# Optimization experiments

Measured on AMD Instinct MI355X. Metric: run time of the kernel, lower is better.

## Reference

```python
import jax, jax.numpy as jnp
import numpy as np

LN_EPS = 1e-5


def _ln(h, g, b):
    mu = h.mean(-1, keepdims=True)
    var = ((h - mu) ** 2).mean(-1, keepdims=True)
    return (h - mu) / jnp.sqrt(var + LN_EPS) * g + b


def setup_inputs() -> dict:
    key = jax.random.key(0)
    ks = jax.random.split(key, 12)
    B, T, Cin, C, D, M = 16, 1024, 512, 1024, 256, 1024
    s = 0.02
    inp = {
        "x": jax.random.normal(ks[0], (B, T, Cin), jnp.float32),
        "masks": jnp.ones((B, T), jnp.float32),
        "W1": jax.random.normal(ks[1], (Cin, C), jnp.float32) * s,
        "g1": jnp.ones((C,), jnp.float32), "b1": jnp.zeros((C,), jnp.float32),
        "W2": jax.random.normal(ks[2], (C, C), jnp.float32) * s,
        "g2": jnp.ones((C,), jnp.float32), "b2": jnp.zeros((C,), jnp.float32),
        "W3": jax.random.normal(ks[3], (C, C), jnp.float32) * s,
        "g3": jnp.ones((C,), jnp.float32), "b3": jnp.zeros((C,), jnp.float32),
        "W4": jax.random.normal(ks[4], (C, C), jnp.float32) * s,
        "g4": jnp.ones((C,), jnp.float32), "b4": jnp.zeros((C,), jnp.float32),
        "W5": jax.random.normal(ks[5], (C, D), jnp.float32) * s,
        "b5": jnp.zeros((D,), jnp.float32),
        # Dirichlet(alpha=100) rows, as in the torch init: rows live on the simplex
        "embedding": jax.random.dirichlet(ks[6], jnp.full((D,), 100.0, jnp.float32), (M,)).astype(jnp.float32),
    }
    return inp


def reference(x, masks, W1, g1, b1, W2, g2, b2, W3, g3, b3, W4, g4, b4, W5, b5, embedding):
    h = jax.nn.relu(_ln(x @ W1, g1, b1))
    h = jax.nn.relu(_ln(h @ W2, g2, b2))
    h = jax.nn.relu(_ln(h @ W3, g3, b3))
    h = jax.nn.relu(_ln(h @ W4, g4, b4))
    z = h @ W5 + b5                              # [B, T, D]
    p = jax.nn.log_softmax(z, axis=-1)           # log-prob features

    B, T, D = p.shape
    p_flat = jax.lax.stop_gradient(p.reshape(-1, D))   # x.detach() in torch
    ep = jnp.exp(p_flat)                               # [N, D]
    # KL(exp(p) || e_m) summed over D, for all codes m:
    #   sum_d exp(p)*(p - log(e_m)) = rowsum(exp(p)*p) - exp(p) @ log(E)^T
    div = (ep * p_flat).sum(-1, keepdims=True) - ep @ jnp.log(embedding).T  # [N, M]
    idx = jnp.argmin(div, axis=-1)                     # [N]
    quant = jax.lax.stop_gradient(embedding[idx].reshape(B, T, D))

    # commitment loss: masked KL(exp(p) || quant.detach())
    kl = (jnp.exp(p) * (p - jnp.log(quant))).sum(-1)   # [B, T]
    loss = 0.25 * (kl * masks).mean(0).sum()

    # straight-through estimator
    q = p + jax.lax.stop_gradient(quant - p)
    return z, q, loss
```

## Files before the change

### kernel.cpp

```cpp
#include <hip/hip_runtime.h>
#include <hip/hip_bf16.h>
#include <stdint.h>

typedef __attribute__((ext_vector_type(4))) float f32x4;
typedef __attribute__((ext_vector_type(2))) float f32x2;
typedef __attribute__((ext_vector_type(8))) __bf16 bf16x8;
typedef __attribute__((ext_vector_type(4))) __bf16 bf16x4;

#define LN_EPS 1e-5f

__device__ __forceinline__ void gload_lds16(const void* g, void* l) {
  __builtin_amdgcn_global_load_lds(
      (__attribute__((address_space(1))) void*)(uintptr_t)g,
      (__attribute__((address_space(3))) void*)(uint32_t)(uintptr_t)l,
      16, 0, 0);
}

__device__ __forceinline__ f32x4 mfma16(bf16x8 a, bf16x8 b, f32x4 c) {
  return __builtin_amdgcn_mfma_f32_16x16x32_bf16(a, b, c, 0, 0, 0);
}

__device__ __forceinline__ void transpose256(const float* __restrict__ W,
                                             __bf16* __restrict__ Wt, int K, int N,
                                             int nt, int kt, float (*t)[33]) {
  int tx = threadIdx.x & 31;
  int ty0 = (threadIdx.x >> 5) * 4;
#pragma unroll
  for (int j = 0; j < 4; ++j)
    t[ty0 + j][tx] = W[(size_t)(kt + ty0 + j) * N + nt + tx];
  __syncthreads();
#pragma unroll
  for (int j = 0; j < 4; ++j)
    Wt[(size_t)(nt + ty0 + j) * K + kt + tx] = (__bf16)t[tx][ty0 + j];
}

__global__ __launch_bounds__(256) void k_prep(
    const float* __restrict__ W1, __bf16* __restrict__ W1t,
    const float* __restrict__ W2, __bf16* __restrict__ W2t,
    const float* __restrict__ W3, __bf16* __restrict__ W3t,
    const float* __restrict__ W4, __bf16* __restrict__ W4t,
    const float* __restrict__ W5, __bf16* __restrict__ W5t,
    const float* __restrict__ emb, __bf16* __restrict__ logE) {
  __shared__ float t[32][33];
  const int b = blockIdx.x;
  if (b < 512) {
    transpose256(W1, W1t, 512, 1024, (b & 31) * 32, (b >> 5) * 32, t);
  } else if (b < 3584) {
    int b3 = b - 512;
    int z = b3 >> 10;
    int b4 = b3 & 1023;
    const float* W = z == 0 ? W2 : (z == 1 ? W3 : W4);
    __bf16* T = z == 0 ? W2t : (z == 1 ? W3t : W4t);
    transpose256(W, T, 1024, 1024, (b4 & 31) * 32, (b4 >> 5) * 32, t);
  } else if (b < 3840) {
    int b5 = b - 3584;
    transpose256(W5, W5t, 1024, 256, (b5 & 7) * 32, (b5 >> 3) * 32, t);
  } else {
    int i = (b - 3840) * 256 + threadIdx.x;
    logE[i] = (__bf16)logf(emb[i] * 256.0f);
  }
}

__device__ __forceinline__ void stats_epilogue(char* lds, f32x4 (&acc)[8][4],
                                               f32x2* __restrict__ outPart,
                                               int bm0) {
  const int tid = threadIdx.x;
  const int lane = tid & 63;
  const int wid = tid >> 6;
  const int wm = wid >> 2, wn = wid & 3;
  const int r0 = (lane >> 4) * 4;
  const int cc = lane & 15;
  __builtin_amdgcn_s_barrier();
  float* stp = (float*)lds;
  float* stq = (float*)(lds + 4096);
#pragma unroll
  for (int mi = 0; mi < 8; ++mi) {
#pragma unroll
    for (int j = 0; j < 4; ++j) {
      float s = 0.f, q = 0.f;
#pragma unroll
      for (int ni = 0; ni < 4; ++ni) {
        float v = acc[mi][ni][j];
        s += v; q += v * v;
      }
#pragma unroll
      for (int d = 1; d < 16; d <<= 1) { s += __shfl_xor(s, d); q += __shfl_xor(q, d); }
      if (cc == 0) {
        int rl = wm * 128 + mi * 16 + r0 + j;
        stp[rl * 4 + wn] = s;
        stq[rl * 4 + wn] = q;
      }
    }
  }
  __syncthreads();
  if (tid < 256) {
    float s = stp[tid * 4] + stp[tid * 4 + 1] + stp[tid * 4 + 2] + stp[tid * 4 + 3];
    float q = stq[tid * 4] + stq[tid * 4 + 1] + stq[tid * 4 + 2] + stq[tid * 4 + 3];
    f32x2 pr; pr[0] = s; pr[1] = q;
    outPart[(size_t)(bm0 + tid) * 4 + blockIdx.y] = pr;
  }
}

__device__ __forceinline__ void gemm256_core(
    const __bf16* __restrict__ A, const __bf16* __restrict__ Bt,
    char* lds, int bm0, int bn0, int K, f32x4 (&acc)[8][4]) {
  const int tid = threadIdx.x;
  const int lane = tid & 63;
  const int wid = tid >> 6;
  const int wm = wid >> 2;
  const int wn = wid & 3;
  const int NT = K >> 6;

  const int slin = tid * 16;
  const int lrow = slin >> 7;
  const int scol = (slin & 127) ^ ((lrow & 7) << 4);
  const char* Ab = (const char*)A;
  const char* Bb = (const char*)Bt;
  const uint32_t rs = (uint32_t)K * 2;

  const int klo = (lane >> 4) * 16;
  const int sw = (lane & 7) << 4;
  const uint32_t kx0 = (uint32_t)(klo ^ sw);
  const uint32_t kx1 = (uint32_t)((64 + klo) ^ sw);
  const uint32_t abase = (uint32_t)(wm * 128 + (lane & 15)) * 128;
  const uint32_t bbase = (uint32_t)(wn * 64 + (lane & 15)) * 128;

#pragma unroll
  for (int i = 0; i < 8; ++i)
#pragma unroll
    for (int j = 0; j < 4; ++j) acc[i][j] = 0.0f;

#define LDSA(buf) (lds + (buf)*32768)
#define LDSB(buf) (lds + 65536 + (buf)*32768)
#define STAGE_A(t, h)                                                              \
  {                                                                                \
    const char* src = Ab + (size_t)(bm0 + (h)*128 + lrow) * rs + ((t) << 7) + scol;\
    char* dst = LDSA((t)&1) + (h)*16384 + slin;                                    \
    gload_lds16(src, dst);                                                         \
    gload_lds16(src + (size_t)64 * rs, dst + 8192);                                \
  }
#define STAGE_B(t, h)                                                              \
  {                                                                                \
    const char* src = Bb + (size_t)(bn0 + (h)*128 + lrow) * rs + ((t) << 7) + scol;\
    char* dst = LDSB((t)&1) + (h)*16384 + slin;                                    \
    gload_lds16(src, dst);                                                         \
    gload_lds16(src + (size_t)64 * rs, dst + 8192);                                \
  }
#define HALF1(Acur, Bcur)                                                          \
  _Pragma("unroll") for (int ni = 0; ni < 4; ++ni) {                               \
    bF[ni][0] = *(const bf16x8*)((Bcur) + bbase + ni * 2048 + kx0);                \
    bF[ni][1] = *(const bf16x8*)((Bcur) + bbase + ni * 2048 + kx1);                \
  }                                                                                \
  {                                                                                \
    bf16x8 aF[4][2];                                                               \
    _Pragma("unroll") for (int mi = 0; mi < 4; ++mi) {                             \
      aF[mi][0] = *(const bf16x8*)((Acur) + abase + mi * 2048 + kx0);              \
      aF[mi][1] = *(const bf16x8*)((Acur) + abase + mi * 2048 + kx1);              \
    }                                                                              \
    __builtin_amdgcn_s_setprio(1);                                                 \
    _Pragma("unroll") for (int mi = 0; mi < 4; ++mi)                               \
        _Pragma("unroll") for (int ni = 0; ni < 4; ++ni) {                         \
          acc[mi][ni] = mfma16(aF[mi][0], bF[ni][0], acc[mi][ni]);                 \
          acc[mi][ni] = mfma16(aF[mi][1], bF[ni][1], acc[mi][ni]);                 \
        }                                                                          \
    __builtin_amdgcn_s_setprio(0);                                                 \
  }
#define HALF2(Acur)                                                                \
  {                                                                                \
    bf16x8 aF[4][2];                                                               \
    _Pragma("unroll") for (int mi = 0; mi < 4; ++mi) {                             \
      aF[mi][0] = *(const bf16x8*)((Acur) + abase + (mi + 4) * 2048 + kx0);        \
      aF[mi][1] = *(const bf16x8*)((Acur) + abase + (mi + 4) * 2048 + kx1);        \
    }                                                                              \
    __builtin_amdgcn_s_setprio(1);                                                 \
    _Pragma("unroll") for (int mi = 0; mi < 4; ++mi)                               \
        _Pragma("unroll") for (int ni = 0; ni < 4; ++ni) {                         \
          acc[mi + 4][ni] = mfma16(aF[mi][0], bF[ni][0], acc[mi + 4][ni]);         \
          acc[mi + 4][ni] = mfma16(aF[mi][1], bF[ni][1], acc[mi + 4][ni]);         \
        }                                                                          \
    __builtin_amdgcn_s_setprio(0);                                                 \
  }

  STAGE_A(0, 0); STAGE_A(0, 1); STAGE_B(0, 0); STAGE_B(0, 1);
  STAGE_B(1, 0); STAGE_B(1, 1);
  asm volatile("s_waitcnt vmcnt(4)");
  __builtin_amdgcn_s_barrier();
  __builtin_amdgcn_sched_barrier(0);

  bf16x8 bF[4][2];
  for (int t = 0; t < NT - 2; ++t) {
    const char* Acur = LDSA(t & 1);
    const char* Bcur = LDSB(t & 1);
    STAGE_A(t + 1, 0); STAGE_A(t + 1, 1);
    HALF1(Acur, Bcur)
    __builtin_amdgcn_s_barrier();
    __builtin_amdgcn_sched_barrier(0);
    STAGE_B(t + 2, 0); STAGE_B(t + 2, 1);
    HALF2(Acur)
    asm volatile("s_waitcnt vmcnt(4)");
    __builtin_amdgcn_s_barrier();
    __builtin_amdgcn_sched_barrier(0);
  }
  {
    const char* Acur = LDSA((NT - 2) & 1);
    const char* Bcur = LDSB((NT - 2) & 1);
    STAGE_A(NT - 1, 0); STAGE_A(NT - 1, 1);
    HALF1(Acur, Bcur)
    __builtin_amdgcn_s_barrier();
    __builtin_amdgcn_sched_barrier(0);
    HALF2(Acur)
    asm volatile("s_waitcnt vmcnt(0)");
    __builtin_amdgcn_s_barrier();
    __builtin_amdgcn_sched_barrier(0);
  }
  {
    const char* Acur = LDSA((NT - 1) & 1);
    const char* Bcur = LDSB((NT - 1) & 1);
    HALF1(Acur, Bcur)
    HALF2(Acur)
  }
#undef STAGE_A
#undef HALF1
#undef HALF2
#undef LDSA
#undef LDSB
#undef STAGE_B
}

__global__ __launch_bounds__(512, 2) void k_gemm256_div(
    const __bf16* __restrict__ A, const __bf16* __restrict__ Bt,
    float* __restrict__ part_val, int* __restrict__ part_idx, int N, int K) {
  __shared__ char lds[131072];
  const int bm0 = blockIdx.x * 256;
  const int bn0 = blockIdx.y * 256;
  f32x4 acc[8][4];
  gemm256_core(A, Bt, lds, bm0, bn0, K, acc);

  const int lane = threadIdx.x & 63;
  const int wid = threadIdx.x >> 6;
  const int wm = wid >> 2, wn = wid & 3;
  const int r0 = (lane >> 4) * 4;
  const int cc = lane & 15;
  const int nch = N >> 6;
  const int chunk = (bn0 >> 6) + wn;
#pragma unroll
  for (int mi = 0; mi < 8; ++mi) {
#pragma unroll
    for (int j = 0; j < 4; ++j) {
      float v = acc[mi][0][j];
      int c = cc;
#pragma unroll
      for (int ni = 1; ni < 4; ++ni) {
        float v2 = acc[mi][ni][j];
        int c2 = ni * 16 + cc;
        if (v2 > v) { v = v2; c = c2; }
      }
#pragma unroll
      for (int d = 1; d < 16; d <<= 1) {
        float ov = __shfl_xor(v, d);
        int oc = __shfl_xor(c, d);
        if (ov > v || (ov == v && oc < c)) { v = ov; c = oc; }
      }
      if (cc == 0) {
        int r = bm0 + wm * 128 + mi * 16 + r0 + j;
        part_val[r * nch + chunk] = v;
        part_idx[r * nch + chunk] = bn0 + wn * 64 + c;
      }
    }
  }
}

__global__ __launch_bounds__(512, 2) void k_gemm256_cvt(
    const float* __restrict__ A, const __bf16* __restrict__ Bt,
    __bf16* __restrict__ O, f32x2* __restrict__ outPart, int N, int K) {
  __shared__ char lds[131072];
  const int tid = threadIdx.x;
  const int lane = tid & 63;
  const int wid = tid >> 6;
  const int wm = wid >> 2;
  const int wn = wid & 3;
  const int bm0 = blockIdx.x * 256;
  const int bn0 = blockIdx.y * 256;
  const int NT = K >> 6;

  const int slin = tid * 16;
  const int lrow = slin >> 7;
  const int scol = (slin & 127) ^ ((lrow & 7) << 4);
  const char* Ab = (const char*)A;
  const char* Bb = (const char*)Bt;
  const uint32_t rsA = (uint32_t)K * 4;
  const uint32_t rs = (uint32_t)K * 2;

  const int klo = (lane >> 4) * 16;
  const int sw = (lane & 7) << 4;
  const uint32_t kx0 = (uint32_t)(klo ^ sw);
  const uint32_t kx1 = (uint32_t)((64 + klo) ^ sw);
  const uint32_t abase = (uint32_t)(wm * 128 + (lane & 15)) * 128;
  const uint32_t bbase = (uint32_t)(wn * 64 + (lane & 15)) * 128;

  const int alrow = tid >> 3;
  const uint32_t acolbF = (uint32_t)(tid & 7) * 32;
  const uint32_t awcol = ((uint32_t)(tid & 7) * 16) ^ (uint32_t)((alrow & 7) << 4);
  f32x4 arf[4][2];

  f32x4 acc[8][4];
#pragma unroll
  for (int i = 0; i < 8; ++i)
#pragma unroll
    for (int j = 0; j < 4; ++j) acc[i][j] = 0.0f;

#define LDSA(buf) (lds + (buf)*32768)
#define LDSB(buf) (lds + 65536 + (buf)*32768)
#define STAGE_B(t, h)                                                              \
  {                                                                                \
    const char* src = Bb + (size_t)(bn0 + (h)*128 + lrow) * rs + ((t) << 7) + scol;\
    char* dst = LDSB((t)&1) + (h)*16384 + slin;                                    \
    gload_lds16(src, dst);                                                         \
    gload_lds16(src + (size_t)64 * rs, dst + 8192);                                \
  }
#define A_ISSUE(t1)                                                               \
  {                                                                               \
    const char* base_ = Ab + (size_t)(bm0 + alrow) * rsA + ((size_t)(t1) << 8) + acolbF; \
    _Pragma("unroll") for (int i = 0; i < 4; ++i) {                               \
      arf[i][0] = *(const f32x4*)(base_ + (size_t)(i * 64) * rsA);                \
      arf[i][1] = *(const f32x4*)(base_ + (size_t)(i * 64) * rsA + 16);           \
    }                                                                             \
  }
#define A_WRITE(t1)                                                               \
  {                                                                               \
    char* wb_ = LDSA((t1)&1);                                                     \
    _Pragma("unroll") for (int i = 0; i < 4; ++i) {                               \
      bf16x8 o;                                                                   \
      _Pragma("unroll") for (int e = 0; e < 4; ++e) {                             \
        o[e] = (__bf16)arf[i][0][e];                                              \
        o[e + 4] = (__bf16)arf[i][1][e];                                          \
      }                                                                           \
      *(bf16x8*)(wb_ + (i >> 1) * 16384 + (alrow + (i & 1) * 64) * 128 + awcol) = o; \
    }                                                                             \
  }
#define HALF1(Acur, Bcur)                                                          \
  _Pragma("unroll") for (int ni = 0; ni < 4; ++ni) {                               \
    bF[ni][0] = *(const bf16x8*)((Bcur) + bbase + ni * 2048 + kx0);                \
    bF[ni][1] = *(const bf16x8*)((Bcur) + bbase + ni * 2048 + kx1);                \
  }                                                                                \
  {                                                                                \
    bf16x8 aF[4][2];                                                               \
    _Pragma("unroll") for (int mi = 0; mi < 4; ++mi) {                             \
      aF[mi][0] = *(const bf16x8*)((Acur) + abase + mi * 2048 + kx0);              \
      aF[mi][1] = *(const bf16x8*)((Acur) + abase + mi * 2048 + kx1);              \
    }                                                                              \
    __builtin_amdgcn_s_setprio(1);                                                 \
    _Pragma("unroll") for (int mi = 0; mi < 4; ++mi)                               \
        _Pragma("unroll") for (int ni = 0; ni < 4; ++ni) {                         \
          acc[mi][ni] = mfma16(aF[mi][0], bF[ni][0], acc[mi][ni]);                 \
          acc[mi][ni] = mfma16(aF[mi][1], bF[ni][1], acc[mi][ni]);                 \
        }                                                                          \
    __builtin_amdgcn_s_setprio(0);                                                 \
  }
#define HALF2(Acur)                                                                \
  {                                                                                \
    bf16x8 aF[4][2];                                                               \
    _Pragma("unroll") for (int mi = 0; mi < 4; ++mi) {                             \
      aF[mi][0] = *(const bf16x8*)((Acur) + abase + (mi + 4) * 2048 + kx0);        \
      aF[mi][1] = *(const bf16x8*)((Acur) + abase + (mi + 4) * 2048 + kx1);        \
    }                                                                              \
    __builtin_amdgcn_s_setprio(1);                                                 \
    _Pragma("unroll") for (int mi = 0; mi < 4; ++mi)                               \
        _Pragma("unroll") for (int ni = 0; ni < 4; ++ni) {                         \
          acc[mi + 4][ni] = mfma16(aF[mi][0], bF[ni][0], acc[mi + 4][ni]);         \
          acc[mi + 4][ni] = mfma16(aF[mi][1], bF[ni][1], acc[mi + 4][ni]);         \
        }                                                                          \
    __builtin_amdgcn_s_setprio(0);                                                 \
  }

  A_ISSUE(0)
  STAGE_B(0, 0); STAGE_B(0, 1); STAGE_B(1, 0); STAGE_B(1, 1);
  asm volatile("s_waitcnt vmcnt(8)");
  A_WRITE(0)
  asm volatile("s_waitcnt vmcnt(4) lgkmcnt(0)");
  __builtin_amdgcn_s_barrier();
  __builtin_amdgcn_sched_barrier(0);

  bf16x8 bF[4][2];
  for (int t = 0; t < NT - 2; ++t) {
    const char* Acur = LDSA(t & 1);
    const char* Bcur = LDSB(t & 1);
    A_ISSUE(t + 1)
    HALF1(Acur, Bcur)
    __builtin_amdgcn_s_barrier();
    __builtin_amdgcn_sched_barrier(0);
    STAGE_B(t + 2, 0); STAGE_B(t + 2, 1);
    HALF2(Acur)
    asm volatile("s_waitcnt vmcnt(4)");
    A_WRITE(t + 1)
    asm volatile("s_waitcnt lgkmcnt(0)");
    __builtin_amdgcn_s_barrier();
    __builtin_amdgcn_sched_barrier(0);
  }
  {
    const char* Acur = LDSA((NT - 2) & 1);
    const char* Bcur = LDSB((NT - 2) & 1);
    A_ISSUE(NT - 1)
    HALF1(Acur, Bcur)
    __builtin_amdgcn_s_barrier();
    __builtin_amdgcn_sched_barrier(0);
    HALF2(Acur)
    asm volatile("s_waitcnt vmcnt(0)");
    A_WRITE(NT - 1)
    asm volatile("s_waitcnt lgkmcnt(0)");
    __builtin_amdgcn_s_barrier();
    __builtin_amdgcn_sched_barrier(0);
  }
  {
    const char* Acur = LDSA((NT - 1) & 1);
    const char* Bcur = LDSB((NT - 1) & 1);
    HALF1(Acur, Bcur)
    HALF2(Acur)
  }
#undef STAGE_B
#undef A_ISSUE
#undef A_WRITE
#undef HALF1
#undef HALF2
#undef LDSA
#undef LDSB

  stats_epilogue(lds, acc, outPart, bm0);

  const int r0 = (lane >> 4) * 4;
  const int cc = lane & 15;
#pragma unroll
  for (int mi = 0; mi < 8; ++mi) {
#pragma unroll
    for (int ni = 0; ni < 4; ++ni) {
      int r = bm0 + wm * 128 + mi * 16 + r0;
      int c = bn0 + wn * 64 + ni * 16 + cc;
#pragma unroll
      for (int j = 0; j < 4; ++j)
        O[(size_t)(r + j) * N + c] = (__bf16)acc[mi][ni][j];
    }
  }
}

__global__ __launch_bounds__(512, 2) void k_gemm256_ln(
    const __bf16* __restrict__ A, const __bf16* __restrict__ Bt,
    __bf16* __restrict__ O, const float* __restrict__ gw,
    const float* __restrict__ bw, const f32x2* __restrict__ inPart,
    f32x2* __restrict__ outPart, int N, int K) {
  __shared__ char lds[139264];
  const int GB = 131072;
  const int tid = threadIdx.x;
  const int lane = tid & 63;
  const int wid = tid >> 6;
  const int wm = wid >> 2;
  const int wn = wid & 3;
  const int bm0 = blockIdx.x * 256;
  const int bn0 = blockIdx.y * 256;
  const int NT = K >> 6;

  const int slin = tid * 16;
  const int lrow = slin >> 7;
  const int scol = (slin & 127) ^ ((lrow & 7) << 4);
  const char* Ab = (const char*)A;
  const char* Bb = (const char*)Bt;
  const uint32_t rs = (uint32_t)K * 2;

  const int klo = (lane >> 4) * 16;
  const int sw = (lane & 7) << 4;
  const uint32_t kx0 = (uint32_t)(klo ^ sw);
  const uint32_t kx1 = (uint32_t)((64 + klo) ^ sw);
  const uint32_t abase = (uint32_t)(wm * 128 + (lane & 15)) * 128;
  const uint32_t bbase = (uint32_t)(wn * 64 + (lane & 15)) * 128;

  const int alrow = tid >> 3;
  const uint32_t acolb = (uint32_t)(tid & 7) * 16;
  const uint32_t awcol = acolb ^ (uint32_t)((alrow & 7) << 4);
  float aS[4], cS[4];
  bf16x8 ar[4];

  f32x4 acc[8][4];
#pragma unroll
  for (int i = 0; i < 8; ++i)
#pragma unroll
    for (int j = 0; j < 4; ++j) acc[i][j] = 0.0f;

#define LDSA(buf) (lds + (buf)*32768)
#define LDSB(buf) (lds + 65536 + (buf)*32768)
#define STAGE_B(t, h)                                                              \
  {                                                                                \
    const char* src = Bb + (size_t)(bn0 + (h)*128 + lrow) * rs + ((t) << 7) + scol;\
    char* dst = LDSB((t)&1) + (h)*16384 + slin;                                    \
    gload_lds16(src, dst);                                                         \
    gload_lds16(src + (size_t)64 * rs, dst + 8192);                                \
  }
#define A_ISSUE(t1)                                                               \
  {                                                                               \
    const char* base_ = Ab + (size_t)(bm0 + alrow) * rs + ((size_t)(t1) << 7) + acolb; \
    ar[0] = *(const bf16x8*)(base_);                                              \
    ar[1] = *(const bf16x8*)(base_ + (size_t)64 * rs);                            \
    ar[2] = *(const bf16x8*)(base_ + (size_t)128 * rs);                           \
    ar[3] = *(const bf16x8*)(base_ + (size_t)192 * rs);                           \
  }
#define A_WRITE(t1)                                                               \
  {                                                                               \
    uint32_t gb_ = GB + (uint32_t)(t1)*256 + (uint32_t)(tid & 7) * 32;            \
    f32x4 g0 = *(const f32x4*)(lds + gb_), g1 = *(const f32x4*)(lds + gb_ + 16);  \
    f32x4 b0 = *(const f32x4*)(lds + gb_ + 4096), b1 = *(const f32x4*)(lds + gb_ + 4112); \
    char* wb_ = LDSA((t1)&1);                                                     \
    _Pragma("unroll") for (int i = 0; i < 4; ++i) {                               \
      bf16x8 v = ar[i], o;                                                        \
      _Pragma("unroll") for (int e = 0; e < 8; ++e) {                             \
        float xv = (float)v[e];                                                   \
        float tt = fmaf(xv, aS[i], cS[i]);                                        \
        float ge = e < 4 ? g0[e] : g1[e - 4];                                     \
        float be = e < 4 ? b0[e] : b1[e - 4];                                     \
        tt = fmaf(tt, ge, be);                                                    \
        o[e] = (__bf16)fmaxf(tt, 0.f);                                            \
      }                                                                           \
      *(bf16x8*)(wb_ + (i >> 1) * 16384 + (alrow + (i & 1) * 64) * 128 + awcol) = o; \
    }                                                                             \
  }

  if (tid < 256) {
    ((f32x4*)(lds + GB))[tid] = ((const f32x4*)gw)[tid];
    ((f32x4*)(lds + GB + 4096))[tid] = ((const f32x4*)bw)[tid];
  }
#pragma unroll
  for (int i = 0; i < 4; ++i) {
    int r = bm0 + (i >> 1) * 128 + (i & 1) * 64 + alrow;
    const f32x4* pp = (const f32x4*)(inPart + (size_t)r * 4);
    f32x4 p0 = pp[0], p1 = pp[1];
    float s = p0[0] + p0[2] + p1[0] + p1[2];
    float q = p0[1] + p0[3] + p1[1] + p1[3];
    float mu = s * (1.0f / 1024.0f);
    float var = q * (1.0f / 1024.0f) - mu * mu;
    float rstd = rsqrtf(var + LN_EPS);
    aS[i] = rstd;
    cS[i] = -mu * rstd;
  }
  __builtin_amdgcn_sched_barrier(0);
  A_ISSUE(0)
  STAGE_B(0, 0); STAGE_B(0, 1); STAGE_B(1, 0); STAGE_B(1, 1);
  __builtin_amdgcn_sched_barrier(0);
  asm volatile("s_waitcnt lgkmcnt(0)");
  __builtin_amdgcn_s_barrier();
  asm volatile("s_waitcnt vmcnt(8)");
  A_WRITE(0)
  asm volatile("s_waitcnt vmcnt(4) lgkmcnt(0)");
  __builtin_amdgcn_s_barrier();
  __builtin_amdgcn_sched_barrier(0);

  for (int t = 0; t < NT; ++t) {
    const char* Acur = LDSA(t & 1);
    const char* Bcur = LDSB(t & 1);

    if (t + 1 < NT) { A_ISSUE(t + 1) }
    bf16x8 bF[4][2];
#pragma unroll
    for (int ni = 0; ni < 4; ++ni) {
      bF[ni][0] = *(const bf16x8*)(Bcur + bbase + ni * 2048 + kx0);
      bF[ni][1] = *(const bf16x8*)(Bcur + bbase + ni * 2048 + kx1);
    }
    {
      bf16x8 aF[4][2];
#pragma unroll
      for (int mi = 0; mi < 4; ++mi) {
        aF[mi][0] = *(const bf16x8*)(Acur + abase + mi * 2048 + kx0);
        aF[mi][1] = *(const bf16x8*)(Acur + abase + mi * 2048 + kx1);
      }
      __builtin_amdgcn_s_setprio(1);
#pragma unroll
      for (int mi = 0; mi < 4; ++mi)
#pragma unroll
        for (int ni = 0; ni < 4; ++ni) {
          acc[mi][ni] = mfma16(aF[mi][0], bF[ni][0], acc[mi][ni]);
          acc[mi][ni] = mfma16(aF[mi][1], bF[ni][1], acc[mi][ni]);
        }
      __builtin_amdgcn_s_setprio(0);
    }
    __builtin_amdgcn_s_barrier();
    __builtin_amdgcn_sched_barrier(0);

    if (t + 2 < NT) { STAGE_B(t + 2, 0); STAGE_B(t + 2, 1); }
    {
      bf16x8 aF[4][2];
#pragma unroll
      for (int mi = 0; mi < 4; ++mi) {
        aF[mi][0] = *(const bf16x8*)(Acur + abase + (mi + 4) * 2048 + kx0);
        aF[mi][1] = *(const bf16x8*)(Acur + abase + (mi + 4) * 2048 + kx1);
      }
      __builtin_amdgcn_s_setprio(1);
#pragma unroll
      for (int mi = 0; mi < 4; ++mi)
#pragma unroll
        for (int ni = 0; ni < 4; ++ni) {
          acc[mi + 4][ni] = mfma16(aF[mi][0], bF[ni][0], acc[mi + 4][ni]);
          acc[mi + 4][ni] = mfma16(aF[mi][1], bF[ni][1], acc[mi + 4][ni]);
        }
      __builtin_amdgcn_s_setprio(0);
    }
    if (t + 1 < NT) {
      if (t + 2 < NT) { asm volatile("s_waitcnt vmcnt(4)"); }
      else            { asm volatile("s_waitcnt vmcnt(0)"); }
      A_WRITE(t + 1)
      asm volatile("s_waitcnt lgkmcnt(0)");
      __builtin_amdgcn_s_barrier();
      __builtin_amdgcn_sched_barrier(0);
    }
  }
#undef STAGE_B
#undef A_ISSUE
#undef A_WRITE
#undef LDSA
#undef LDSB

  stats_epilogue(lds, acc, outPart, bm0);

  const int r0 = (lane >> 4) * 4;
  const int cc = lane & 15;
#pragma unroll
  for (int mi = 0; mi < 8; ++mi) {
#pragma unroll
    for (int ni = 0; ni < 4; ++ni) {
      int r = bm0 + wm * 128 + mi * 16 + r0;
      int c = bn0 + wn * 64 + ni * 16 + cc;
#pragma unroll
      for (int j = 0; j < 4; ++j)
        O[(size_t)(r + j) * N + c] = (__bf16)acc[mi][ni][j];
    }
  }
}

__global__ __launch_bounds__(256) void k_gemm_sm(
    const __bf16* __restrict__ A, const __bf16* __restrict__ Bt,
    const float* __restrict__ gw, const float* __restrict__ bw,
    const f32x2* __restrict__ inPart, const float* __restrict__ bias,
    float* __restrict__ z, __bf16* __restrict__ ep, float* __restrict__ sm) {
  const int K = 1024;
  __shared__ char lds[49152];
  const int GBS = 40960;
  char* ldsA = lds;
  char* ldsB = lds + 8192;
  const int tid = threadIdx.x;
  const int lane = tid & 63;
  const int wn = tid >> 6;
  const int bm0 = blockIdx.x * 64;
  const char* Ab = (const char*)A;
  const char* Bb = (const char*)Bt;
  const uint32_t rs = (uint32_t)K * 2;
  const int cc = lane & 15;

  ((f32x4*)(lds + GBS))[tid] = ((const f32x4*)gw)[tid];
  ((f32x4*)(lds + GBS + 4096))[tid] = ((const f32x4*)bw)[tid];

  const int ar0 = tid >> 3;
  float aS[2], cS[2];
#pragma unroll
  for (int i = 0; i < 2; ++i) {
    int r = bm0 + ar0 + i * 32;
    const f32x4* pp = (const f32x4*)(inPart + (size_t)r * 4);
    f32x4 p0 = pp[0], p1 = pp[1];
    float s = p0[0] + p0[2] + p1[0] + p1[2];
    float q = p0[1] + p0[3] + p1[1] + p1[3];
    float mu = s * (1.0f / 1024.0f);
    float var = q * (1.0f / 1024.0f) - mu * mu;
    float rstd = rsqrtf(var + LN_EPS);
    aS[i] = rstd; cS[i] = -mu * rstd;
  }
  const uint32_t acolb = (uint32_t)(tid & 7) * 16;
  const uint32_t awcol = acolb ^ (uint32_t)((ar0 & 7) << 4);

  uint32_t ra[2][4], rb[2][4];
  {
    const int sww = (lane & 7) << 4;
    const int gk = lane & 48;
#pragma unroll
    for (int kk = 0; kk < 2; ++kk) {
#pragma unroll
      for (int i = 0; i < 4; ++i) {
        uint32_t kb = (uint32_t)((kk * 64 + gk) ^ sww);
        ra[kk][i] = (uint32_t)(i * 16 + cc) * 128 + kb;
        rb[kk][i] = (uint32_t)(wn * 64 + i * 16 + cc) * 128 + kb;
      }
    }
  }

  f32x4 acc[4][4];
#pragma unroll
  for (int i = 0; i < 4; ++i)
#pragma unroll
    for (int j = 0; j < 4; ++j) acc[i][j] = 0.0f;

  for (int k0 = 0; k0 < K; k0 += 64) {
    __syncthreads();
    const char* abase_ = Ab + (size_t)(bm0 + ar0) * rs + (size_t)k0 * 2 + acolb;
    bf16x8 a0 = *(const bf16x8*)abase_;
    bf16x8 a1 = *(const bf16x8*)(abase_ + (size_t)32 * rs);
#pragma unroll
    for (int i = 0; i < 8; ++i) {
      int lin = i * 4096 + tid * 16;
      int row = lin >> 7;
      int col = (lin & 127) ^ ((row & 7) << 4);
      gload_lds16(Bb + (size_t)row * rs + k0 * 2 + col, ldsB + lin);
    }
    asm volatile("s_waitcnt vmcnt(8)");
    {
      uint32_t gb_ = GBS + (uint32_t)k0 * 4 + (uint32_t)(tid & 7) * 32;
      f32x4 g0 = *(const f32x4*)(lds + gb_), g1 = *(const f32x4*)(lds + gb_ + 16);
      f32x4 b0 = *(const f32x4*)(lds + gb_ + 4096), b1 = *(const f32x4*)(lds + gb_ + 4112);
      bf16x8 o0, o1;
#pragma unroll
      for (int e = 0; e < 8; ++e) {
        float ge = e < 4 ? g0[e] : g1[e - 4];
        float be = e < 4 ? b0[e] : b1[e - 4];
        float t0 = fmaf(fmaf((float)a0[e], aS[0], cS[0]), ge, be);
        float t1 = fmaf(fmaf((float)a1[e], aS[1], cS[1]), ge, be);
        o0[e] = (__bf16)fmaxf(t0, 0.f);
        o1[e] = (__bf16)fmaxf(t1, 0.f);
      }
      *(bf16x8*)(ldsA + ar0 * 128 + awcol) = o0;
      *(bf16x8*)(ldsA + (ar0 + 32) * 128 + awcol) = o1;
    }
    __syncthreads();
#pragma unroll
    for (int kk = 0; kk < 2; ++kk) {
      bf16x8 af[4], bfv[4];
#pragma unroll
      for (int i = 0; i < 4; ++i) af[i] = *(const bf16x8*)(ldsA + ra[kk][i]);
#pragma unroll
      for (int i = 0; i < 4; ++i) bfv[i] = *(const bf16x8*)(ldsB + rb[kk][i]);
#pragma unroll
      for (int mi = 0; mi < 4; ++mi)
#pragma unroll
        for (int ni = 0; ni < 4; ++ni)
          acc[mi][ni] = mfma16(af[mi], bfv[ni], acc[mi][ni]);
    }
  }

  __syncthreads();
  float* stm = (float*)lds;
  float* sts = (float*)(lds + 1024);
  float* rowm = (float*)(lds + 2048);
  float* rows_ = (float*)(lds + 2304);

  const int r0 = (lane >> 4) * 4;
  float bvv[4];
#pragma unroll
  for (int ni = 0; ni < 4; ++ni) bvv[ni] = bias[wn * 64 + ni * 16 + cc];

#pragma unroll
  for (int mi = 0; mi < 4; ++mi) {
#pragma unroll
    for (int j = 0; j < 4; ++j) {
      float m = -3.4e38f;
#pragma unroll
      for (int ni = 0; ni < 4; ++ni) m = fmaxf(m, acc[mi][ni][j] + bvv[ni]);
#pragma unroll
      for (int d = 1; d < 16; d <<= 1) m = fmaxf(m, __shfl_xor(m, d));
      if (cc == 0) stm[wn * 64 + mi * 16 + r0 + j] = m;
    }
  }
  __syncthreads();
  if (tid < 64) {
    float m = fmaxf(fmaxf(stm[tid], stm[64 + tid]), fmaxf(stm[128 + tid], stm[192 + tid]));
    rowm[tid] = m;
  }
  __syncthreads();
#pragma unroll
  for (int mi = 0; mi < 4; ++mi) {
#pragma unroll
    for (int j = 0; j < 4; ++j) {
      int r = mi * 16 + r0 + j;
      float m = rowm[r];
      float s = 0.f;
#pragma unroll
      for (int ni = 0; ni < 4; ++ni) s += expf(acc[mi][ni][j] + bvv[ni] - m);
#pragma unroll
      for (int d = 1; d < 16; d <<= 1) s += __shfl_xor(s, d);
      if (cc == 0) sts[wn * 64 + r] = s;
    }
  }
  __syncthreads();
  if (tid < 64) {
    float s = sts[tid] + sts[64 + tid] + sts[128 + tid] + sts[192 + tid];
    rows_[tid] = s;
    sm[bm0 + tid] = rowm[tid] + logf(s);
  }
  __syncthreads();
#pragma unroll
  for (int mi = 0; mi < 4; ++mi) {
#pragma unroll
    for (int j = 0; j < 4; ++j) {
      int r = mi * 16 + r0 + j;
      float m = rowm[r];
      float inv = 1.0f / rows_[r];
      float* zp = z + (size_t)(bm0 + r) * 256;
      __bf16* epp = ep + (size_t)(bm0 + r) * 256;
#pragma unroll
      for (int ni = 0; ni < 4; ++ni) {
        int c = wn * 64 + ni * 16 + cc;
        float zz = acc[mi][ni][j] + bvv[ni];
        zp[c] = zz;
        epp[c] = (__bf16)(expf(zz - m) * inv);
      }
    }
  }
}

__global__ __launch_bounds__(256) void k_final(
    const float* __restrict__ part_val, const int* __restrict__ part_idx,
    const float* __restrict__ z, const float* __restrict__ sm,
    const float* __restrict__ emb, const float* __restrict__ masks,
    float* __restrict__ q, float* __restrict__ blockloss) {
  __shared__ float ls[4];
  int lane = threadIdx.x & 63;
  int w = threadIdx.x >> 6;
  int row = blockIdx.x * 4 + w;
  float v = -3.4e38f;
  int c = 0x7fffffff;
  if (lane < 16) { v = part_val[row * 16 + lane]; c = part_idx[row * 16 + lane]; }
#pragma unroll
  for (int d = 1; d < 16; d <<= 1) {
    float ov = __shfl_xor(v, d);
    int oc = __shfl_xor(c, d);
    if (ov > v || (ov == v && oc < c)) { v = ov; c = oc; }
  }
  int code = __shfl(c, 0);
  f32x4 ev = ((const f32x4*)(emb + (size_t)code * 256))[lane];
  ((f32x4*)(q + (size_t)row * 256))[lane] = ev;
  f32x4 zv = ((const f32x4*)(z + (size_t)row * 256))[lane];
  float smr = sm[row];
  float kl = 0.f;
#pragma unroll
  for (int j = 0; j < 4; ++j) {
    float pj = zv[j] - smr;
    kl += expf(pj) * (pj - logf(ev[j]));
  }
#pragma unroll
  for (int d = 1; d < 64; d <<= 1) kl += __shfl_xor(kl, d);
  if (lane == 0) ls[w] = kl * masks[row];
  __syncthreads();
  if (threadIdx.x == 0) blockloss[blockIdx.x] = ls[0] + ls[1] + ls[2] + ls[3];
}

__global__ __launch_bounds__(256) void k_loss_reduce(const float* __restrict__ bl,
                                                     float* __restrict__ out) {
  __shared__ float s[256];
  float a = 0.f;
#pragma unroll
  for (int i = 0; i < 16; ++i) a += bl[threadIdx.x + i * 256];
  s[threadIdx.x] = a;
  __syncthreads();
  for (int st = 128; st > 0; st >>= 1) {
    if (threadIdx.x < st) s[threadIdx.x] += s[threadIdx.x + st];
    __syncthreads();
  }
  if (threadIdx.x == 0) out[0] = s[0] * (0.25f / 16.0f);
}

extern "C" void kernel_launch(void* const* d_in, const int* in_sizes, int n_in,
                              void* d_out, int out_size, void* d_ws, size_t ws_size,
                              hipStream_t stream) {
  const float* x = (const float*)d_in[0];
  const float* masks = (const float*)d_in[1];
  const float* W1 = (const float*)d_in[2];
  const float* g1 = (const float*)d_in[3];
  const float* b1 = (const float*)d_in[4];
  const float* W2 = (const float*)d_in[5];
  const float* g2 = (const float*)d_in[6];
  const float* b2 = (const float*)d_in[7];
  const float* W3 = (const float*)d_in[8];
  const float* g3 = (const float*)d_in[9];
  const float* b3 = (const float*)d_in[10];
  const float* W4 = (const float*)d_in[11];
  const float* g4 = (const float*)d_in[12];
  const float* b4 = (const float*)d_in[13];
  const float* W5 = (const float*)d_in[14];
  const float* b5 = (const float*)d_in[15];
  const float* emb = (const float*)d_in[16];

  const int M = 16384;
  char* ws = (char*)d_ws;
  __bf16* bufA = (__bf16*)(ws);
  __bf16* bufB = (__bf16*)(ws + (32ull << 20));
  __bf16* W1t = (__bf16*)(ws + (64ull << 20));
  __bf16* W2t = (__bf16*)(ws + (65ull << 20));
  __bf16* W3t = (__bf16*)(ws + (67ull << 20));
  __bf16* W4t = (__bf16*)(ws + (69ull << 20));
  __bf16* W5t = (__bf16*)(ws + (71ull << 20));
  __bf16* logE = (__bf16*)(ws + (72ull << 20));
  float* part_val = (float*)(ws + (73ull << 20));
  int* part_idx = (int*)(ws + (74ull << 20));
  float* blockloss = (float*)(ws + (75ull << 20));
  float* sm = (float*)(ws + (76ull << 20));
  f32x2* partA = (f32x2*)(ws + (77ull << 20));
  f32x2* partB = (f32x2*)(ws + (78ull << 20));
  __bf16* ep = (__bf16*)(ws + (16ull << 20));

  float* z = (float*)d_out;
  float* q = z + (size_t)M * 256;
  float* lossp = z + 2ull * M * 256;

  k_prep<<<4864, 256, 0, stream>>>(W1, W1t, W2, W2t, W3, W3t, W4, W4t,
                                   W5, W5t, emb, logE);
  k_gemm256_cvt<<<dim3(64, 4), 512, 0, stream>>>(x, W1t, bufA, partA, 1024, 512);
  k_gemm256_ln<<<dim3(64, 4), 512, 0, stream>>>(bufA, W2t, bufB, g1, b1, partA, partB, 1024, 1024);
  k_gemm256_ln<<<dim3(64, 4), 512, 0, stream>>>(bufB, W3t, bufA, g2, b2, partB, partA, 1024, 1024);
  k_gemm256_ln<<<dim3(64, 4), 512, 0, stream>>>(bufA, W4t, bufB, g3, b3, partA, partB, 1024, 1024);
  k_gemm_sm<<<256, 256, 0, stream>>>(bufB, W5t, g4, b4, partB, b5, z, ep, sm);
  k_gemm256_div<<<dim3(64, 4), 512, 0, stream>>>(ep, logE, part_val, part_idx, 1024, 256);
  k_final<<<4096, 256, 0, stream>>>(part_val, part_idx, z, sm, emb, masks, q, blockloss);
  k_loss_reduce<<<1, 256, 0, stream>>>(blockloss, lossp);
}
```

Before: 247.9 us.

## Double-buffer B tiles in softmax GEMM and fold loss reduce into final kernel

The W5 GEMM kernel now keeps two LDS buffers for the B tile and prefetches tile t+1 while computing tile t, replacing the per-iteration syncthreads pattern with explicit barriers. This hides global-to-LDS latency at the cost of more LDS (80KB), which may lower occupancy. Separately, the final kernel uses an atomic counter so the last block does the loss reduction, removing one kernel launch. The counter is reset in the prep kernel.

```diff
diff --git a/kernel.cpp b/kernel.cpp
--- a/kernel.cpp
+++ b/kernel.cpp
@@ -40,9 +40,11 @@
     const float* __restrict__ W3, __bf16* __restrict__ W3t,
     const float* __restrict__ W4, __bf16* __restrict__ W4t,
     const float* __restrict__ W5, __bf16* __restrict__ W5t,
-    const float* __restrict__ emb, __bf16* __restrict__ logE) {
+    const float* __restrict__ emb, __bf16* __restrict__ logE,
+    int* __restrict__ counter) {
   __shared__ float t[32][33];
   const int b = blockIdx.x;
+  if (b == 0 && threadIdx.x == 0) *counter = 0;
   if (b < 512) {
     transpose256(W1, W1t, 512, 1024, (b & 31) * 32, (b >> 5) * 32, t);
   } else if (b < 3584) {
@@ -637,10 +639,9 @@
     const f32x2* __restrict__ inPart, const float* __restrict__ bias,
     float* __restrict__ z, __bf16* __restrict__ ep, float* __restrict__ sm) {
   const int K = 1024;
-  __shared__ char lds[49152];
-  const int GBS = 40960;
+  __shared__ char lds[81920];
+  const int GBS = 73728;
   char* ldsA = lds;
-  char* ldsB = lds + 8192;
   const int tid = threadIdx.x;
   const int lane = tid & 63;
   const int wn = tid >> 6;
@@ -691,21 +692,31 @@
 #pragma unroll
     for (int j = 0; j < 4; ++j) acc[i][j] = 0.0f;
 
-  for (int k0 = 0; k0 < K; k0 += 64) {
-    __syncthreads();
-    const char* abase_ = Ab + (size_t)(bm0 + ar0) * rs + (size_t)k0 * 2 + acolb;
+#define STAGE_BS(t)                                                               \
+  {                                                                               \
+    char* bdst = lds + 8192 + ((t)&1) * 32768;                                    \
+    _Pragma("unroll") for (int i = 0; i < 8; ++i) {                               \
+      int lin = i * 4096 + tid * 16;                                              \
+      int row = lin >> 7;                                                         \
+      int col = (lin & 127) ^ ((row & 7) << 4);                                   \
+      gload_lds16(Bb + (size_t)row * rs + ((size_t)(t) << 7) + col, bdst + lin);  \
+    }                                                                             \
+  }
+
+  STAGE_BS(0)
+  asm volatile("s_waitcnt lgkmcnt(0)");
+  __builtin_amdgcn_s_barrier();
+  __builtin_amdgcn_sched_barrier(0);
+
+  for (int t = 0; t < 16; ++t) {
+    const char* abase_ = Ab + (size_t)(bm0 + ar0) * rs + ((size_t)t << 7) + acolb;
     bf16x8 a0 = *(const bf16x8*)abase_;
     bf16x8 a1 = *(const bf16x8*)(abase_ + (size_t)32 * rs);
-#pragma unroll
-    for (int i = 0; i < 8; ++i) {
-      int lin = i * 4096 + tid * 16;
-      int row = lin >> 7;
-      int col = (lin & 127) ^ ((row & 7) << 4);
-      gload_lds16(Bb + (size_t)row * rs + k0 * 2 + col, ldsB + lin);
-    }
-    asm volatile("s_waitcnt vmcnt(8)");
+    if (t + 1 < 16) { STAGE_BS(t + 1) }
+    if (t + 1 < 16) { asm volatile("s_waitcnt vmcnt(8)"); }
+    else            { asm volatile("s_waitcnt vmcnt(0)"); }
     {
-      uint32_t gb_ = GBS + (uint32_t)k0 * 4 + (uint32_t)(tid & 7) * 32;
+      uint32_t gb_ = GBS + (uint32_t)t * 256 + (uint32_t)(tid & 7) * 32;
       f32x4 g0 = *(const f32x4*)(lds + gb_), g1 = *(const f32x4*)(lds + gb_ + 16);
       f32x4 b0 = *(const f32x4*)(lds + gb_ + 4096), b1 = *(const f32x4*)(lds + gb_ + 4112);
       bf16x8 o0, o1;
@@ -721,21 +732,29 @@
       *(bf16x8*)(ldsA + ar0 * 128 + awcol) = o0;
       *(bf16x8*)(ldsA + (ar0 + 32) * 128 + awcol) = o1;
     }
-    __syncthreads();
-#pragma unroll
-    for (int kk = 0; kk < 2; ++kk) {
-      bf16x8 af[4], bfv[4];
-#pragma unroll
-      for (int i = 0; i < 4; ++i) af[i] = *(const bf16x8*)(ldsA + ra[kk][i]);
-#pragma unroll
-      for (int i = 0; i < 4; ++i) bfv[i] = *(const bf16x8*)(ldsB + rb[kk][i]);
-#pragma unroll
-      for (int mi = 0; mi < 4; ++mi)
-#pragma unroll
-        for (int ni = 0; ni < 4; ++ni)
-          acc[mi][ni] = mfma16(af[mi], bfv[ni], acc[mi][ni]);
-    }
-  }
+    asm volatile("s_waitcnt lgkmcnt(0)");
+    __builtin_amdgcn_s_barrier();
+    __builtin_amdgcn_sched_barrier(0);
+    {
+      const char* Bcur = lds + 8192 + (t & 1) * 32768;
+#pragma unroll
+      for (int kk = 0; kk < 2; ++kk) {
+        bf16x8 af[4], bfv[4];
+#pragma unroll
+        for (int i = 0; i < 4; ++i) af[i] = *(const bf16x8*)(ldsA + ra[kk][i]);
+#pragma unroll
+        for (int i = 0; i < 4; ++i) bfv[i] = *(const bf16x8*)(Bcur + rb[kk][i]);
+#pragma unroll
+        for (int mi = 0; mi < 4; ++mi)
+#pragma unroll
+          for (int ni = 0; ni < 4; ++ni)
+            acc[mi][ni] = mfma16(af[mi], bfv[ni], acc[mi][ni]);
+      }
+    }
+    __builtin_amdgcn_s_barrier();
+    __builtin_amdgcn_sched_barrier(0);
+  }
+#undef STAGE_BS
 
   __syncthreads();
   float* stm = (float*)lds;
@@ -811,8 +830,11 @@
     const float* __restrict__ part_val, const int* __restrict__ part_idx,
     const float* __restrict__ z, const float* __restrict__ sm,
     const float* __restrict__ emb, const float* __restrict__ masks,
-    float* __restrict__ q, float* __restrict__ blockloss) {
+    float* __restrict__ q, float* __restrict__ blockloss,
+    int* __restrict__ counter, float* __restrict__ lossp) {
   __shared__ float ls[4];
+  __shared__ int lastflag;
+  __shared__ float red[256];
   int lane = threadIdx.x & 63;
   int w = threadIdx.x >> 6;
   int row = blockIdx.x * 4 + w;
@@ -840,22 +862,26 @@
   for (int d = 1; d < 64; d <<= 1) kl += __shfl_xor(kl, d);
   if (lane == 0) ls[w] = kl * masks[row];
   __syncthreads();
-  if (threadIdx.x == 0) blockloss[blockIdx.x] = ls[0] + ls[1] + ls[2] + ls[3];
-}
-
-__global__ __launch_bounds__(256) void k_loss_reduce(const float* __restrict__ bl,
-                                                     float* __restrict__ out) {
-  __shared__ float s[256];
-  float a = 0.f;
-#pragma unroll
-  for (int i = 0; i < 16; ++i) a += bl[threadIdx.x + i * 256];
-  s[threadIdx.x] = a;
+  if (threadIdx.x == 0) {
+    blockloss[blockIdx.x] = ls[0] + ls[1] + ls[2] + ls[3];
+    __threadfence();
+    int prev = atomicAdd(counter, 1);
+    lastflag = (prev == 4095) ? 1 : 0;
+  }
   __syncthreads();
-  for (int st = 128; st > 0; st >>= 1) {
-    if (threadIdx.x < st) s[threadIdx.x] += s[threadIdx.x + st];
+  if (lastflag) {
+    __threadfence();
+    float a = 0.f;
+#pragma unroll
+    for (int i = 0; i < 16; ++i) a += blockloss[threadIdx.x + i * 256];
+    red[threadIdx.x] = a;
     __syncthreads();
-  }
-  if (threadIdx.x == 0) out[0] = s[0] * (0.25f / 16.0f);
+    for (int st = 128; st > 0; st >>= 1) {
+      if (threadIdx.x < st) red[threadIdx.x] += red[threadIdx.x + st];
+      __syncthreads();
+    }
+    if (threadIdx.x == 0) lossp[0] = red[0] * (0.25f / 16.0f);
+  }
 }
 
 extern "C" void kernel_launch(void* const* d_in, const int* in_sizes, int n_in,
@@ -892,6 +918,7 @@
   float* part_val = (float*)(ws + (73ull << 20));
   int* part_idx = (int*)(ws + (74ull << 20));
   float* blockloss = (float*)(ws + (75ull << 20));
+  int* counter = (int*)(ws + (75ull << 20) + 16384);
   float* sm = (float*)(ws + (76ull << 20));
   f32x2* partA = (f32x2*)(ws + (77ull << 20));
   f32x2* partB = (f32x2*)(ws + (78ull << 20));
@@ -902,13 +929,13 @@
   float* lossp = z + 2ull * M * 256;
 
   k_prep<<<4864, 256, 0, stream>>>(W1, W1t, W2, W2t, W3, W3t, W4, W4t,
-                                   W5, W5t, emb, logE);
+                                   W5, W5t, emb, logE, counter);
   k_gemm256_cvt<<<dim3(64, 4), 512, 0, stream>>>(x, W1t, bufA, partA, 1024, 512);
   k_gemm256_ln<<<dim3(64, 4), 512, 0, stream>>>(bufA, W2t, bufB, g1, b1, partA, partB, 1024, 1024);
   k_gemm256_ln<<<dim3(64, 4), 512, 0, stream>>>(bufB, W3t, bufA, g2, b2, partB, partA, 1024, 1024);
   k_gemm256_ln<<<dim3(64, 4), 512, 0, stream>>>(bufA, W4t, bufB, g3, b3, partA, partB, 1024, 1024);
   k_gemm_sm<<<256, 256, 0, stream>>>(bufB, W5t, g4, b4, partB, b5, z, ep, sm);
   k_gemm256_div<<<dim3(64, 4), 512, 0, stream>>>(ep, logE, part_val, part_idx, 1024, 256);
-  k_final<<<4096, 256, 0, stream>>>(part_val, part_idx, z, sm, emb, masks, q, blockloss);
-  k_loss_reduce<<<1, 256, 0, stream>>>(blockloss, lossp);
-}
+  k_final<<<4096, 256, 0, stream>>>(part_val, part_idx, z, sm, emb, masks, q,
+                                    blockloss, counter, lossp);
+}
```

New measurement: 340.6 us. 37.4% more time.
